# Kernel tuning notes

Hardware: AMD Instinct MI355X
Metric: run time of the kernel (lower is better)

The kernel has to match this reference:

```python
import jax, jax.numpy as jnp
import numpy as np

B, S, D, H, DH = 2, 4096, 768, 12, 64
BS, NB, L, FF, VOCAB = 16, 256, 2, 3072, 50358
SCALE = 1.0 / np.sqrt(DH)


def _ln(x, g, b, eps=1e-12):
    m = jnp.mean(x, -1, keepdims=True)
    v = jnp.var(x, -1, keepdims=True)
    return (x - m) * jax.lax.rsqrt(v + eps) * g + b


def _make_key_block_idx(seed=0):
    rng = np.random.default_rng(seed)
    idx = np.zeros((NB, 7), np.int32)
    allb = np.arange(NB)
    for i in range(NB):
        req = sorted({0, NB - 1, max(i - 1, 0), i, min(i + 1, NB - 1)})
        pool = np.setdiff1d(allb, req)
        extra = rng.choice(pool, size=7 - len(req), replace=False)
        idx[i] = np.concatenate([req, extra])
    return jnp.asarray(idx)


def _sparse_attn(q, k, v, key_idx):
    # q,k,v: [B,H,NB,BS,DH]; key_idx: [NB,7]
    kg = k[:, :, key_idx].reshape(B, H, NB, 7 * BS, DH)  # gather key blocks
    vg = v[:, :, key_idx].reshape(B, H, NB, 7 * BS, DH)
    s = jnp.einsum('bhnqd,bhnkd->bhnqk', q, kg) * SCALE
    o = jnp.einsum('bhnqk,bhnkd->bhnqd', jax.nn.softmax(s, -1), vg)
    # first/last query blocks: full (global) attention over all keys
    qe = q[:, :, jnp.array([0, NB - 1])]                 # [B,H,2,BS,DH]
    kf = k.reshape(B, H, S, DH)
    vf = v.reshape(B, H, S, DH)
    se = jnp.einsum('bhgqd,bhkd->bhgqk', qe, kf) * SCALE
    oe = jnp.einsum('bhgqk,bhkd->bhgqd', jax.nn.softmax(se, -1), vf)
    o = o.at[:, :, 0].set(oe[:, :, 0]).at[:, :, NB - 1].set(oe[:, :, 1])
    # [B,H,NB,BS,DH] -> [B,S,D]
    return o.transpose(0, 2, 3, 1, 4).reshape(B, S, D)


def setup_inputs():
    key = jax.random.key(0)
    ks = iter(jax.random.split(key, 24))
    n = lambda sh, s=0.02: jax.random.normal(next(ks), sh, jnp.float32) * s
    inp = {
        'input_ids': jax.random.randint(next(ks), (B, S), 0, VOCAB),
        'key_block_idx': _make_key_block_idx(),
        'embed': n((VOCAB, D)),
        'Wqkv': n((L, D, 3 * D)), 'bqkv': jnp.zeros((L, 3 * D)),
        'Wo': n((L, D, D)), 'bo': jnp.zeros((L, D)),
        'ln1_g': jnp.ones((L, D)), 'ln1_b': jnp.zeros((L, D)),
        'Wff1': n((L, D, FF)), 'bff1': jnp.zeros((L, FF)),
        'Wff2': n((L, FF, D)), 'bff2': jnp.zeros((L, D)),
        'ln2_g': jnp.ones((L, D)), 'ln2_b': jnp.zeros((L, D)),
        'Wp': n((D, D)), 'bp': jnp.zeros((D,)),
        'start_w': jax.random.normal(next(ks), (D,)),
        'end_w': jax.random.normal(next(ks), (D,)),
        'd1_W': n((D, 20)), 'd1_b': jnp.zeros((20,)),
        'd2_W': n((20, 2)), 'd2_b': jnp.zeros((2,)),
    }
    return inp


def reference(input_ids, key_block_idx, embed, Wqkv, bqkv, Wo, bo, ln1_g, ln1_b,
              Wff1, bff1, Wff2, bff2, ln2_g, ln2_b, Wp, bp, start_w, end_w,
              d1_W, d1_b, d2_W, d2_b):
    x = embed[input_ids]                                  # [B,S,D]
    for l in range(L):
        qkv = x @ Wqkv[l] + bqkv[l]
        q, k, v = jnp.split(qkv, 3, axis=-1)
        blk = lambda t: t.reshape(B, NB, BS, H, DH).transpose(0, 3, 1, 2, 4)
        a = _sparse_attn(blk(q), blk(k), blk(v), key_block_idx)
        x = _ln(x + a @ Wo[l] + bo[l], ln1_g[l], ln1_b[l])
        h = jax.nn.gelu(x @ Wff1[l] + bff1[l]) @ Wff2[l] + bff2[l]
        x = _ln(x + h, ln2_g[l], ln2_b[l])
    pool = jnp.tanh(x[:, 0] @ Wp + bp)                    # BigBird pooler
    start_probs = jax.nn.softmax(x @ start_w, -1)         # [B,S]
    end_probs = jax.nn.softmax(x @ end_w, -1)
    d = (pool[0] @ d1_W + d1_b) @ d2_W + d2_b             # no ReLU, as in source
    disc = jax.nn.softmax(d, -1)
    return start_probs, end_probs, disc
```

## Files before the change

kernel.cpp:

```cpp
#include <hip/hip_runtime.h>
#include <hip/hip_bf16.h>
#include <math.h>

#define B_   2
#define S_   4096
#define D_   768
#define H_   12
#define DH_  64
#define BS_  16
#define NB_  256
#define FF_  3072
#define BT_  (B_ * S_)
#define SCALE_F 0.125f

#define NSPLIT 32
#define TILES_PER_SPLIT (NB_ / NSPLIT)
#define NEDGE (B_ * H_ * 2)
#define NSPARSE (B_ * H_ * NB_)
#define NXCD 8

typedef _Float16 f16x8 __attribute__((ext_vector_type(8)));
typedef _Float16 f16x4 __attribute__((ext_vector_type(4)));
typedef _Float16 f16x2 __attribute__((ext_vector_type(2)));
typedef float    f32x4 __attribute__((ext_vector_type(4)));
typedef float    f32x16 __attribute__((ext_vector_type(16)));

#define DKS 8
#define DKC (D_ / DKS)

#define MFMA_PV(a, b, c) __builtin_amdgcn_mfma_f32_16x16x16f16(a, b, c, 0, 0, 0)

__device__ __forceinline__ int xcd_swz(int bid, int nwg)
{
    int q = nwg / NXCD;
    return (bid % NXCD) * q + bid / NXCD;
}

#define GLD16(gp, lp) __builtin_amdgcn_global_load_lds( \
    (const __attribute__((address_space(1))) void*)(gp), \
    (__attribute__((address_space(3))) void*)(lp), 16, 0, 0)

__device__ __forceinline__ float fast_tanh(float z)
{
    float az = fabsf(z);
    float t = __expf(-2.0f * az);
    float r = (1.0f - t) / (1.0f + t);
    return z < 0.f ? -r : r;
}

__device__ __forceinline__ float gelu_tanh(float v)
{
    float v3 = v * v * v;
    return 0.5f * v * (1.0f + fast_tanh(0.79788456080286535588f * (v + 0.044715f * v3)));
}

struct WSeg { const float* src; _Float16* dst; int K; int N; int start; };
struct WSegs { WSeg s[8]; int total; };

__global__ __launch_bounds__(256) void prep_all(
    WSegs segs, const int* __restrict__ ids, const float* __restrict__ emb,
    _Float16* __restrict__ xh)
{
    int bt = blockIdx.x;
    int t = threadIdx.x;
    if (bt < segs.total) {
        __shared__ float tile[32][33];
        int si = 0;
#pragma unroll
        for (int u = 1; u < 8; ++u)
            if (bt >= segs.s[u].start) si = u;
        const WSeg& sg = segs.s[si];
        int tid = bt - sg.start;
        int tn = sg.N >> 5;
        int n0 = (tid % tn) * 32;
        int k0 = (tid / tn) * 32;

        {
            int r = t >> 3, c = (t & 7) * 4;
            f32x4 v = *(const f32x4*)&sg.src[(size_t)(k0 + r) * sg.N + n0 + c];
            tile[r][c + 0] = v[0];
            tile[r][c + 1] = v[1];
            tile[r][c + 2] = v[2];
            tile[r][c + 3] = v[3];
        }
        __syncthreads();
        {
            int r = t >> 3, c = (t & 7) * 4;
            f16x4 o;
            o[0] = (_Float16)tile[c + 0][r];
            o[1] = (_Float16)tile[c + 1][r];
            o[2] = (_Float16)tile[c + 2][r];
            o[3] = (_Float16)tile[c + 3][r];
            *(f16x4*)&sg.dst[(size_t)(n0 + r) * sg.K + k0 + c] = o;
        }
    } else {
        int row = bt - segs.total;
        int id = ids[row];
        const float* src = emb + (size_t)id * D_;
        _Float16* dst16 = xh + (size_t)row * D_;
        for (int d = t; d < D_; d += 256)
            dst16[d] = (_Float16)src[d];
    }
}

template<int MI, int DBUF, int ACT, int OUT16>
__global__ __launch_bounds__(256) void gemm_f16(
    const _Float16* __restrict__ A, const _Float16* __restrict__ Wt,
    const float* __restrict__ bias, void* __restrict__ Cp,
    int M, int N, int K, int NT128)
{
    constexpr int BM = MI * 64;
    constexpr int QA = 2 * MI;
    constexpr int ASZ = BM * 64;
    constexpr int BSZ = 128 * 64;

    __shared__ __attribute__((aligned(16))) _Float16 As[(DBUF ? 2 : 1) * ASZ];
    __shared__ __attribute__((aligned(16))) _Float16 Bs[(DBUF ? 2 : 1) * BSZ];

    int t = threadIdx.x;
    int w = t >> 6, l = t & 63;
    int swz = xcd_swz(blockIdx.x, gridDim.x);
    int bm = (swz / NT128) * BM, bn = (swz % NT128) * 128;
    int wr = (w >> 1) * (MI * 32), wc = (w & 1) * 64;

    f32x16 acc[MI][2];
#pragma unroll
    for (int i = 0; i < MI; ++i)
#pragma unroll
        for (int j = 0; j < 2; ++j)
#pragma unroll
            for (int r = 0; r < 16; ++r) acc[i][j][r] = 0.f;

    const _Float16* gA[QA];
    const _Float16* gB[4];
#pragma unroll
    for (int q = 0; q < QA; ++q) {
        int m = w * QA + q;
        int row = m * 8 + (l >> 3);
        int sc = (l & 7) ^ (row & 7);
        gA[q] = A + (size_t)(bm + row) * K + sc * 8;
    }
#pragma unroll
    for (int q = 0; q < 4; ++q) {
        int m = w * 4 + q;
        int row = m * 8 + (l >> 3);
        int sc = (l & 7) ^ (row & 7);
        gB[q] = Wt + (size_t)(bn + row) * K + sc * 8;
    }

    int aoff[4][MI], boff[4][2];
#pragma unroll
    for (int kk = 0; kk < 4; ++kk) {
        int ch = (kk * 2 + (l >> 5)) ^ (l & 7);
#pragma unroll
        for (int i = 0; i < MI; ++i)
            aoff[kk][i] = (wr + i * 32 + (l & 31)) * 64 + ch * 8;
#pragma unroll
        for (int j = 0; j < 2; ++j)
            boff[kk][j] = (wc + j * 32 + (l & 31)) * 64 + ch * 8;
    }

#define STAGE_(BUF, K0)                                                   \
    {                                                                     \
        _Float16* ab_ = As + (BUF) * ASZ;                                 \
        _Float16* bb_ = Bs + (BUF) * BSZ;                                 \
        _Pragma("unroll")                                                 \
        for (int q = 0; q < QA; ++q)                                      \
            GLD16(gA[q] + (K0), ab_ + (w * QA + q) * 512);                \
        _Pragma("unroll")                                                 \
        for (int q = 0; q < 4; ++q)                                       \
            GLD16(gB[q] + (K0), bb_ + (w * 4 + q) * 512);                 \
    }

#define COMPUTE_(BUF)                                                     \
    {                                                                     \
        const _Float16* ab_ = As + (BUF) * ASZ;                           \
        const _Float16* bb_ = Bs + (BUF) * BSZ;                           \
        _Pragma("unroll")                                                 \
        for (int kk = 0; kk < 4; ++kk) {                                  \
            f16x8 af[MI], bf[2];                                          \
            _Pragma("unroll")                                             \
            for (int i = 0; i < MI; ++i)                                  \
                af[i] = *(const f16x8*)(ab_ + aoff[kk][i]);               \
            _Pragma("unroll")                                             \
            for (int j = 0; j < 2; ++j)                                   \
                bf[j] = *(const f16x8*)(bb_ + boff[kk][j]);               \
            _Pragma("unroll")                                             \
            for (int i = 0; i < MI; ++i)                                  \
                _Pragma("unroll")                                         \
                for (int j = 0; j < 2; ++j)                               \
                    acc[i][j] = __builtin_amdgcn_mfma_f32_32x32x16_f16(   \
                        af[i], bf[j], acc[i][j], 0, 0, 0);                \
        }                                                                 \
    }

    if (DBUF) {
        STAGE_(0, 0);
        __syncthreads();
        int cur = 0;
#pragma unroll 2
        for (int k0 = 0; k0 < K; k0 += 64) {
            if (k0 + 64 < K) STAGE_(cur ^ 1, k0 + 64);
            COMPUTE_(cur);
            __syncthreads();
            cur ^= 1;
        }
    } else {
        for (int k0 = 0; k0 < K; k0 += 64) {
            STAGE_(0, k0);
            __syncthreads();
            COMPUTE_(0);
            __syncthreads();
        }
    }
#undef STAGE_
#undef COMPUTE_

#pragma unroll
    for (int i = 0; i < MI; ++i) {
#pragma unroll
        for (int j = 0; j < 2; ++j) {
            int col = bn + wc + j * 32 + (l & 31);
            float bv = bias[col];
#pragma unroll
            for (int rg = 0; rg < 4; ++rg) {
                int row0 = bm + wr + i * 32 + 8 * rg + 4 * (l >> 5);
#pragma unroll
                for (int r = 0; r < 4; ++r) {
                    float v = acc[i][j][rg * 4 + r] + bv;
                    if (ACT) v = gelu_tanh(v);
                    if (OUT16)
                        ((_Float16*)Cp)[(size_t)(row0 + r) * N + col] = (_Float16)v;
                    else
                        ((float*)Cp)[(size_t)(row0 + r) * N + col] = v;
                }
            }
        }
    }
}

template<int NT, bool EDGE>
__device__ __forceinline__ void attn_wave(
    const _Float16* __restrict__ qkv, const int* __restrict__ key_idx,
    _Float16* __restrict__ outp, float* __restrict__ pm,
    float* __restrict__ pl, float* __restrict__ pacc,
    int b, int h, int n, int split, int be,
    _Float16 (*vq)[24])
{
    int l = threadIdx.x & 63;
    int q = l & 15;
    int g = l >> 4;

    const _Float16* qp = qkv + ((size_t)(b * S_ + n * BS_ + q)) * (3 * D_) + h * DH_ + g * 8;
    f16x8 qf0 = *(const f16x8*)qp;
    f16x8 qf1 = *(const f16x8*)(qp + 32);

    float m_old = -1e30f, lsum = 0.f;
    f32x4 o[4];
#pragma unroll
    for (int db = 0; db < 4; ++db) o[db] = (f32x4){0.f, 0.f, 0.f, 0.f};

#pragma unroll 1
    for (int jj = 0; jj < NT; ++jj) {
        int kb = EDGE ? (split * NT + jj) : key_idx[n * 7 + jj];
        const _Float16* kvrow = qkv + ((size_t)(b * S_ + kb * BS_ + q)) * (3 * D_);

        f16x8 kf0 = *(const f16x8*)(kvrow + D_ + h * DH_ + g * 8);
        f16x8 kf1 = *(const f16x8*)(kvrow + D_ + h * DH_ + g * 8 + 32);

        {
            const _Float16* vp = kvrow + 2 * D_ + h * DH_ + g * 16;
            f16x8 v0 = *(const f16x8*)vp;
            f16x8 v1 = *(const f16x8*)(vp + 8);
#pragma unroll
            for (int u = 0; u < 8; ++u) vq[g * 16 + u][q] = v0[u];
#pragma unroll
            for (int u = 0; u < 8; ++u) vq[g * 16 + 8 + u][q] = v1[u];
        }

        __builtin_amdgcn_s_setprio(1);
        f32x4 sc = (f32x4){0.f, 0.f, 0.f, 0.f};
        sc = __builtin_amdgcn_mfma_f32_16x16x32_f16(kf0, qf0, sc, 0, 0, 0);
        sc = __builtin_amdgcn_mfma_f32_16x16x32_f16(kf1, qf1, sc, 0, 0, 0);
#pragma unroll
        for (int r = 0; r < 4; ++r) sc[r] *= SCALE_F;

        float tm = fmaxf(fmaxf(sc[0], sc[1]), fmaxf(sc[2], sc[3]));
        tm = fmaxf(tm, __shfl_xor(tm, 16, 64));
        tm = fmaxf(tm, __shfl_xor(tm, 32, 64));
        float m_new = fmaxf(m_old, tm);

        float pr[4];
        float rs = 0.f;
#pragma unroll
        for (int r = 0; r < 4; ++r) { pr[r] = __expf(sc[r] - m_new); rs += pr[r]; }
        rs += __shfl_xor(rs, 16, 64);
        rs += __shfl_xor(rs, 32, 64);

        float corr = __expf(m_old - m_new);
        lsum = lsum * corr + rs;
        m_old = m_new;

        float cq[4];
#pragma unroll
        for (int r = 0; r < 4; ++r) cq[r] = __shfl(corr, g * 4 + r, 64);
#pragma unroll
        for (int db = 0; db < 4; ++db)
#pragma unroll
            for (int r = 0; r < 4; ++r) o[db][r] *= cq[r];

        f16x4 pa;
#pragma unroll
        for (int r = 0; r < 4; ++r) pa[r] = (_Float16)pr[r];

#pragma unroll
        for (int db = 0; db < 4; ++db) {
            f16x4 vb = *(const f16x4*)&vq[db * 16 + q][g * 4];
            o[db] = MFMA_PV(pa, vb, o[db]);
        }
        __builtin_amdgcn_s_setprio(0);
    }

    if (EDGE) {
        int base16 = (be * NSPLIT + split) * 16;
        if (l < 16) { pm[base16 + l] = m_old; pl[base16 + l] = lsum; }
#pragma unroll
        for (int db = 0; db < 4; ++db)
#pragma unroll
            for (int r = 0; r < 4; ++r)
                pacc[(size_t)(base16 + g * 4 + r) * 64 + db * 16 + q] = o[db][r];
    } else {
        float linv[4];
#pragma unroll
        for (int r = 0; r < 4; ++r) linv[r] = 1.f / __shfl(lsum, g * 4 + r, 64);
#pragma unroll
        for (int r = 0; r < 4; ++r) {
            _Float16* dst = outp + ((size_t)(b * S_ + n * BS_ + g * 4 + r)) * D_ + h * DH_ + q;
#pragma unroll
            for (int db = 0; db < 4; ++db)
                dst[db * 16] = (_Float16)(o[db][r] * linv[r]);
        }
    }
}

__global__ __launch_bounds__(256) void attn_fused(
    const _Float16* __restrict__ qkv, const int* __restrict__ key_idx,
    _Float16* __restrict__ outp, float* __restrict__ pm,
    float* __restrict__ pl, float* __restrict__ pacc)
{
    __shared__ __attribute__((aligned(16))) _Float16 vqs[4][64][24];

    int w = threadIdx.x >> 6;
    int bi = xcd_swz(blockIdx.x, gridDim.x) * 4 + w;

    if (bi < NSPARSE) {
        int n = bi % NB_;
        if (n == 0 || n == NB_ - 1) return;
        int h = (bi / NB_) % H_;
        int b = bi / (NB_ * H_);
        attn_wave<7, false>(qkv, key_idx, outp, nullptr, nullptr, nullptr,
                            b, h, n, 0, 0, vqs[w]);
    } else {
        int ei = bi - NSPARSE;
        int split = ei % NSPLIT;
        int be = ei / NSPLIT;
        int e = be & 1;
        int h = (be >> 1) % H_;
        int b = be / (2 * H_);
        int n = e ? (NB_ - 1) : 0;
        attn_wave<TILES_PER_SPLIT, true>(qkv, nullptr, nullptr, pm, pl, pacc,
                                         b, h, n, split, be, vqs[w]);
    }
}

__global__ __launch_bounds__(256) void attn_edge_combine(
    const float* __restrict__ pm, const float* __restrict__ pl,
    const float* __restrict__ pacc, _Float16* __restrict__ outp)
{
    int be = blockIdx.x;
    int e = be & 1;
    int h = (be >> 1) % H_;
    int b = be / (2 * H_);
    int n = e ? (NB_ - 1) : 0;

    int t = threadIdx.x;
    int i = t >> 4;
    int c = t & 15;

    float M = -1e30f;
#pragma unroll 4
    for (int s = 0; s < NSPLIT; ++s)
        M = fmaxf(M, pm[(be * NSPLIT + s) * 16 + i]);

    float L = 0.f;
    float acc[4] = {0.f, 0.f, 0.f, 0.f};
    for (int s = 0; s < NSPLIT; ++s) {
        int ps = (be * NSPLIT + s) * 16 + i;
        float wgt = __expf(pm[ps] - M);
        L += pl[ps] * wgt;
#pragma unroll
        for (int u = 0; u < 4; ++u) acc[u] += pacc[(size_t)ps * 64 + c * 4 + u] * wgt;
    }

    float inv = 1.f / L;
    _Float16* dst = outp + ((size_t)(b * S_ + n * BS_ + i)) * D_ + h * DH_ + c * 4;
#pragma unroll
    for (int u = 0; u < 4; ++u) dst[u] = (_Float16)(acc[u] * inv);
}

template<int WRITE32>
__global__ __launch_bounds__(256) void add_ln_kernel(
    _Float16* __restrict__ xh, const _Float16* __restrict__ g,
    const float* __restrict__ gamma, const float* __restrict__ beta,
    float* __restrict__ x32)
{
    int row = blockIdx.x;
    int t = threadIdx.x;
    _Float16* xr = xh + (size_t)row * D_;
    const _Float16* gr = g + (size_t)row * D_;

    float v[3];
    float s = 0.f, s2 = 0.f;
#pragma unroll
    for (int r = 0; r < 3; ++r) {
        int d = t + 256 * r;
        v[r] = (float)xr[d] + (float)gr[d];
        s += v[r];
        s2 += v[r] * v[r];
    }
#pragma unroll
    for (int off = 32; off; off >>= 1) {
        s  += __shfl_xor(s, off, 64);
        s2 += __shfl_xor(s2, off, 64);
    }
    __shared__ float sA[4], sB[4];
    int wave = t >> 6, lane = t & 63;
    if (lane == 0) { sA[wave] = s; sB[wave] = s2; }
    __syncthreads();
    s  = sA[0] + sA[1] + sA[2] + sA[3];
    s2 = sB[0] + sB[1] + sB[2] + sB[3];
    float mean = s * (1.0f / D_);
    float var = s2 * (1.0f / D_) - mean * mean;
    float rstd = rsqrtf(var + 1e-12f);
#pragma unroll
    for (int r = 0; r < 3; ++r) {
        int d = t + 256 * r;
        float o = (v[r] - mean) * rstd * gamma[d] + beta[d];
        xr[d] = (_Float16)o;
        if (WRITE32) x32[(size_t)row * D_ + d] = o;
    }
}

__global__ __launch_bounds__(256) void heads_fused(
    const float* __restrict__ x, const float* __restrict__ sw,
    const float* __restrict__ ew, const float* __restrict__ Wp,
    float* __restrict__ sl, float* __restrict__ el,
    float* __restrict__ partial)
{
    int bi = blockIdx.x;
    int t = threadIdx.x;
    if (bi < 2048) {
        int wave = t >> 6, lane = t & 63;
        int row = bi * 4 + wave;
        const float* xr = x + (size_t)row * D_;
        float a = 0.f, e = 0.f;
        for (int d = lane; d < D_; d += 64) {
            float xv = xr[d];
            a += xv * sw[d];
            e += xv * ew[d];
        }
#pragma unroll
        for (int off = 32; off; off >>= 1) {
            a += __shfl_xor(a, off, 64);
            e += __shfl_xor(e, off, 64);
        }
        if (lane == 0) { sl[row] = a; el[row] = e; }
    } else {
        int ei = bi - 2048;
        int jb = ei % 3;
        int ks = ei / 3;
        int j = jb * 256 + t;
        int k0 = ks * DKC;

        __shared__ float xs[DKC];
        if (t < DKC) xs[t] = x[k0 + t];
        __syncthreads();

        float s = 0.f;
#pragma unroll 8
        for (int kk = 0; kk < DKC; ++kk)
            s += xs[kk] * Wp[(size_t)(k0 + kk) * D_ + j];
        partial[ks * D_ + j] = s;
    }
}

__global__ __launch_bounds__(256) void final_fused(
    const float* __restrict__ sl, const float* __restrict__ el,
    const float* __restrict__ partial, const float* __restrict__ bp,
    const float* __restrict__ d1W, const float* __restrict__ d1b,
    const float* __restrict__ d2W, const float* __restrict__ d2b,
    float* __restrict__ outp)
{
    int r = blockIdx.x;
    int t = threadIdx.x;
    if (r < 4) {
        const float* src = (r < 2 ? sl : el) + (size_t)(r & 1) * S_;
        float* dst = outp + (r < 2 ? 0 : BT_) + (size_t)(r & 1) * S_;
        int wave = t >> 6, lane = t & 63;
        __shared__ float sm[4], ss[4];

        float m = -1e30f;
        for (int k = t; k < S_; k += 256) m = fmaxf(m, src[k]);
#pragma unroll
        for (int off = 32; off; off >>= 1) m = fmaxf(m, __shfl_xor(m, off, 64));
        if (lane == 0) sm[wave] = m;
        __syncthreads();
        m = fmaxf(fmaxf(sm[0], sm[1]), fmaxf(sm[2], sm[3]));

        float s = 0.f;
        for (int k = t; k < S_; k += 256) s += __expf(src[k] - m);
#pragma unroll
        for (int off = 32; off; off >>= 1) s += __shfl_xor(s, off, 64);
        if (lane == 0) ss[wave] = s;
        __syncthreads();
        s = ss[0] + ss[1] + ss[2] + ss[3];

        float inv = 1.f / s;
        for (int k = t; k < S_; k += 256) dst[k] = __expf(src[k] - m) * inv;
    } else {
        __shared__ float pool[D_];
        __shared__ float h1[20];
        float* out2 = outp + 2 * BT_;
        for (int j = t; j < D_; j += 256) {
            float s = bp[j];
#pragma unroll
            for (int ks = 0; ks < DKS; ++ks) s += partial[ks * D_ + j];
            pool[j] = tanhf(s);
        }
        __syncthreads();
        if (t < 20) {
            float s = d1b[t];
            for (int k = 0; k < D_; ++k) s += pool[k] * d1W[k * 20 + t];
            h1[t] = s;
        }
        __syncthreads();
        if (t == 0) {
            float d0 = d2b[0], d1v = d2b[1];
#pragma unroll
            for (int u = 0; u < 20; ++u) {
                d0  += h1[u] * d2W[u * 2 + 0];
                d1v += h1[u] * d2W[u * 2 + 1];
            }
            float m = fmaxf(d0, d1v);
            float e0 = __expf(d0 - m), e1 = __expf(d1v - m);
            float inv = 1.f / (e0 + e1);
            out2[0] = e0 * inv;
            out2[1] = e1 * inv;
        }
    }
}

extern "C" void kernel_launch(void* const* d_in, const int* in_sizes, int n_in,
                              void* d_out, int out_size, void* d_ws, size_t ws_size,
                              hipStream_t stream)
{
    const int*   ids   = (const int*)d_in[0];
    const int*   kbi   = (const int*)d_in[1];
    const float* emb   = (const float*)d_in[2];
    const float* Wqkv  = (const float*)d_in[3];
    const float* bqkv  = (const float*)d_in[4];
    const float* Wo    = (const float*)d_in[5];
    const float* bo    = (const float*)d_in[6];
    const float* ln1g  = (const float*)d_in[7];
    const float* ln1b  = (const float*)d_in[8];
    const float* Wff1  = (const float*)d_in[9];
    const float* bff1  = (const float*)d_in[10];
    const float* Wff2  = (const float*)d_in[11];
    const float* bff2  = (const float*)d_in[12];
    const float* ln2g  = (const float*)d_in[13];
    const float* ln2b  = (const float*)d_in[14];
    const float* Wp    = (const float*)d_in[15];
    const float* bp    = (const float*)d_in[16];
    const float* sw    = (const float*)d_in[17];
    const float* ew    = (const float*)d_in[18];
    const float* d1W   = (const float*)d_in[19];
    const float* d1b   = (const float*)d_in[20];
    const float* d2W   = (const float*)d_in[21];
    const float* d2b   = (const float*)d_in[22];
    float* outp = (float*)d_out;

    float* ws   = (float*)d_ws;
    float* x    = ws;
    float* xbf  = x   + (size_t)BT_ * D_;
    float* r1f  = xbf + (size_t)BT_ * D_ / 2;
    float* abf  = r1f + (size_t)BT_ * FF_ / 2;
    float* r2   = abf + (size_t)BT_ * D_ / 2;
    float* wtf  = r2  + (size_t)BT_ * D_;
    float* sl   = wtf + 7077888;
    float* el   = sl  + BT_;
    float* dpar = el  + BT_;

    _Float16* xh    = (_Float16*)xbf;
    _Float16* qkv16 = (_Float16*)r1f;
    _Float16* h16   = (_Float16*)r1f;
    _Float16* ab    = (_Float16*)abf;
    float* pm   = r2;
    float* pl   = r2 + NEDGE * NSPLIT * 16;
    float* pacc = pl + NEDGE * NSPLIT * 16;
    _Float16* g16 = (_Float16*)r2;

    _Float16* Wt    = (_Float16*)wtf;
    _Float16* WqkvT = Wt;
    _Float16* WoT   = WqkvT + (size_t)2 * 2304 * 768;
    _Float16* Wff1T = WoT   + (size_t)2 * 768 * 768;
    _Float16* Wff2T = Wff1T + (size_t)2 * 3072 * 768;

    WSegs segs;
    int start = 0;
    for (int l = 0; l < 2; ++l) {
        int base = l * 4;
        segs.s[base + 0] = { Wqkv + (size_t)l * 768 * 2304,
                             WqkvT + (size_t)l * 2304 * 768, 768, 2304, start };
        start += (2304 / 32) * (768 / 32);
        segs.s[base + 1] = { Wo + (size_t)l * 768 * 768,
                             WoT + (size_t)l * 768 * 768, 768, 768, start };
        start += (768 / 32) * (768 / 32);
        segs.s[base + 2] = { Wff1 + (size_t)l * 768 * 3072,
                             Wff1T + (size_t)l * 3072 * 768, 768, 3072, start };
        start += (3072 / 32) * (768 / 32);
        segs.s[base + 3] = { Wff2 + (size_t)l * 3072 * 768,
                             Wff2T + (size_t)l * 768 * 3072, 3072, 768, start };
        start += (768 / 32) * (3072 / 32);
    }
    segs.total = start;

    prep_all<<<segs.total + BT_, 256, 0, stream>>>(segs, ids, emb, xh);

    for (int l = 0; l < 2; ++l) {
        gemm_f16<2,0,0,1><<<(BT_/128) * (2304/128), 256, 0, stream>>>(
            xh, WqkvT + (size_t)l * 2304 * 768, bqkv + (size_t)l * 3 * D_,
            qkv16, BT_, 3 * D_, D_, 2304/128);
        attn_fused<<<(NSPARSE + NEDGE * NSPLIT) / 4, 256, 0, stream>>>(
            qkv16, kbi, ab, pm, pl, pacc);
        attn_edge_combine<<<NEDGE, 256, 0, stream>>>(pm, pl, pacc, ab);
        gemm_f16<1,1,0,1><<<(BT_/64) * (768/128), 256, 0, stream>>>(
            ab, WoT + (size_t)l * 768 * 768, bo + (size_t)l * D_,
            g16, BT_, D_, D_, 768/128);
        add_ln_kernel<0><<<BT_, 256, 0, stream>>>(
            xh, g16, ln1g + (size_t)l * D_, ln1b + (size_t)l * D_, nullptr);
        gemm_f16<2,0,1,1><<<(BT_/128) * (3072/128), 256, 0, stream>>>(
            xh, Wff1T + (size_t)l * 3072 * 768, bff1 + (size_t)l * FF_,
            h16, BT_, FF_, D_, 3072/128);
        gemm_f16<1,1,0,1><<<(BT_/64) * (768/128), 256, 0, stream>>>(
            h16, Wff2T + (size_t)l * 768 * 3072, bff2 + (size_t)l * D_,
            g16, BT_, D_, FF_, 768/128);
        if (l == 1)
            add_ln_kernel<1><<<BT_, 256, 0, stream>>>(
                xh, g16, ln2g + (size_t)l * D_, ln2b + (size_t)l * D_, x);
        else
            add_ln_kernel<0><<<BT_, 256, 0, stream>>>(
                xh, g16, ln2g + (size_t)l * D_, ln2b + (size_t)l * D_, nullptr);
    }

    heads_fused<<<2048 + 3 * DKS, 256, 0, stream>>>(x, sw, ew, Wp, sl, el, dpar);
    final_fused<<<5, 256, 0, stream>>>(sl, el, dpar, bp, d1W, d1b, d2W, d2b, outp);
}
```

Before: 551.3 us.

## Load GEMM weight fragments directly from global memory, bypassing LDS staging

The B (weight) tile is no longer staged through shared memory. Each wave now reads its MFMA B fragments straight from global memory inside the compute loop. This removes the LDS footprint and LDS traffic for weights, which could raise occupancy. In exchange, every wave issues uncoalesced 16-byte global loads that sit on the MFMA critical path with no prefetch, and weight rows are refetched by each wave instead of being shared.

New measurement: 874.7 us. 1.59x slower.

```diff
diff --git a/kernel.cpp b/kernel.cpp
--- a/kernel.cpp
+++ b/kernel.cpp
@@ -112,10 +112,8 @@
     constexpr int BM = MI * 64;
     constexpr int QA = 2 * MI;
     constexpr int ASZ = BM * 64;
-    constexpr int BSZ = 128 * 64;
 
     __shared__ __attribute__((aligned(16))) _Float16 As[(DBUF ? 2 : 1) * ASZ];
-    __shared__ __attribute__((aligned(16))) _Float16 Bs[(DBUF ? 2 : 1) * BSZ];
 
     int t = threadIdx.x;
     int w = t >> 6, l = t & 63;
@@ -132,7 +130,6 @@
             for (int r = 0; r < 16; ++r) acc[i][j][r] = 0.f;
 
     const _Float16* gA[QA];
-    const _Float16* gB[4];
 #pragma unroll
     for (int q = 0; q < QA; ++q) {
         int m = w * QA + q;
@@ -140,42 +137,29 @@
         int sc = (l & 7) ^ (row & 7);
         gA[q] = A + (size_t)(bm + row) * K + sc * 8;
     }
-#pragma unroll
-    for (int q = 0; q < 4; ++q) {
-        int m = w * 4 + q;
-        int row = m * 8 + (l >> 3);
-        int sc = (l & 7) ^ (row & 7);
-        gB[q] = Wt + (size_t)(bn + row) * K + sc * 8;
-    }
-
-    int aoff[4][MI], boff[4][2];
+
+    const _Float16* gWb = Wt + (size_t)(bn + wc + (l & 31)) * K + (l >> 5) * 8;
+
+    int aoff[4][MI];
 #pragma unroll
     for (int kk = 0; kk < 4; ++kk) {
         int ch = (kk * 2 + (l >> 5)) ^ (l & 7);
 #pragma unroll
         for (int i = 0; i < MI; ++i)
             aoff[kk][i] = (wr + i * 32 + (l & 31)) * 64 + ch * 8;
-#pragma unroll
-        for (int j = 0; j < 2; ++j)
-            boff[kk][j] = (wc + j * 32 + (l & 31)) * 64 + ch * 8;
     }
 
 #define STAGE_(BUF, K0)                                                   \
     {                                                                     \
         _Float16* ab_ = As + (BUF) * ASZ;                                 \
-        _Float16* bb_ = Bs + (BUF) * BSZ;                                 \
         _Pragma("unroll")                                                 \
         for (int q = 0; q < QA; ++q)                                      \
             GLD16(gA[q] + (K0), ab_ + (w * QA + q) * 512);                \
-        _Pragma("unroll")                                                 \
-        for (int q = 0; q < 4; ++q)                                       \
-            GLD16(gB[q] + (K0), bb_ + (w * 4 + q) * 512);                 \
-    }
-
-#define COMPUTE_(BUF)                                                     \
+    }
+
+#define COMPUTE_(BUF, K0)                                                 \
     {                                                                     \
         const _Float16* ab_ = As + (BUF) * ASZ;                           \
-        const _Float16* bb_ = Bs + (BUF) * BSZ;                           \
         _Pragma("unroll")                                                 \
         for (int kk = 0; kk < 4; ++kk) {                                  \
             f16x8 af[MI], bf[2];                                          \
@@ -184,7 +168,8 @@
                 af[i] = *(const f16x8*)(ab_ + aoff[kk][i]);               \
             _Pragma("unroll")                                             \
             for (int j = 0; j < 2; ++j)                                   \
-                bf[j] = *(const f16x8*)(bb_ + boff[kk][j]);               \
+                bf[j] = *(const f16x8*)(gWb + (size_t)j * 32 * K +        \
+                                        (K0) + kk * 16);                  \
             _Pragma("unroll")                                             \
             for (int i = 0; i < MI; ++i)                                  \
                 _Pragma("unroll")                                         \
@@ -201,7 +186,7 @@
 #pragma unroll 2
         for (int k0 = 0; k0 < K; k0 += 64) {
             if (k0 + 64 < K) STAGE_(cur ^ 1, k0 + 64);
-            COMPUTE_(cur);
+            COMPUTE_(cur, k0);
             __syncthreads();
             cur ^= 1;
         }
@@ -209,7 +194,7 @@
         for (int k0 = 0; k0 < K; k0 += 64) {
             STAGE_(0, k0);
             __syncthreads();
-            COMPUTE_(0);
+            COMPUTE_(0, k0);
             __syncthreads();
         }
     }
```
